# Performance work log

Hardware: AMD Instinct MI355X
Metric: run time of the kernel (lower is better)

Reference implementation:

```python
import jax, jax.numpy as jnp
import numpy as np

IN_F = 4096
OUT_F = 11008
GROUP_SIZE = 128
BITS = 4
PACK = 32 // BITS  # 8 uint4 nibbles per int32


def _unpack_uint4(packed):
    # packed: (rows, cols) int32 -> (rows, cols*8) int32 nibbles in [0,15]
    shifts = (jnp.arange(PACK, dtype=jnp.int32) * BITS)[None, None, :]
    nib = (packed[:, :, None] >> shifts) & 15
    return nib.reshape(packed.shape[0], packed.shape[1] * PACK)


def _dequant(qweight, qzeros, scales):
    # Mirrors torch.ops.hpu.convert_from_uint4: w = (uint4 - zp) * scale,
    # group-wise along the in_features dimension (rows).
    w = _unpack_uint4(qweight).astype(scales.dtype)          # (IN_F, OUT_F)
    zp = _unpack_uint4(qzeros).astype(scales.dtype)          # (n_groups, OUT_F)
    sc_full = jnp.repeat(scales, GROUP_SIZE, axis=0)          # (IN_F, OUT_F)
    zp_full = jnp.repeat(zp, GROUP_SIZE, axis=0)              # (IN_F, OUT_F)
    return (w - zp_full) * sc_full


def setup_inputs() -> dict:
    key = jax.random.key(0)
    k1, k2, k3, k4 = jax.random.split(key, 4)
    n_groups = IN_F // GROUP_SIZE
    inp = jax.random.normal(k1, (2, 2048, IN_F), dtype=jnp.float32)
    qweight = jax.random.randint(k2, (IN_F, OUT_F // PACK), 0, 2147483647, dtype=jnp.int32)
    qzeros = jax.random.randint(k3, (n_groups, OUT_F // PACK), 0, 2147483647, dtype=jnp.int32)
    scales = jax.random.uniform(k4, (n_groups, OUT_F), dtype=jnp.float32) * 0.01 + 1e-3
    return {"input": inp, "qweight": qweight, "qzeros": qzeros, "scales": scales}


def reference(input, qweight, qzeros, scales):
    weight = _dequant(qweight, qzeros, scales)                # (IN_F, OUT_F)
    out = jnp.einsum('bsi,io->bso', input, weight)            # (B, S, OUT_F)
    return out.astype(input.dtype)
```

## Files before the change

kernel.cpp:

```cpp
#include <hip/hip_runtime.h>
#include <stdint.h>

#define IN_F   4096
#define OUT_F  11008
#define QCOLS  (OUT_F / 8)
#define NGRP   32
#define M_TOT  4096

typedef __attribute__((ext_vector_type(8))) short short8;
typedef __attribute__((ext_vector_type(4))) float floatx4;

__device__ __forceinline__ short f2bf(float f) {
    union { float f; uint32_t u; } v; v.f = f;
    uint32_t u = v.u;
    u += 0x7FFFu + ((u >> 16) & 1u);
    return (short)(u >> 16);
}

__global__ __launch_bounds__(256)
void dequant_kernel(const int* __restrict__ qw, const int* __restrict__ qz,
                    const float* __restrict__ scl, short* __restrict__ wt)
{
    const int t    = blockIdx.x * 256 + threadIdx.x;
    const int c    = t % QCOLS;
    const int kblk = t / QCOLS;
    const int k0   = kblk << 5;
    const int g    = kblk >> 2;

    uint32_t q[32];
    const int* qp = qw + (size_t)k0 * QCOLS + c;
    #pragma unroll
    for (int kk = 0; kk < 32; ++kk) q[kk] = (uint32_t)qp[(size_t)kk * QCOLS];

    const uint32_t z = (uint32_t)qz[g * QCOLS + c];
    const float* sp = scl + (size_t)g * OUT_F + c * 8;
    const float4 s0 = *(const float4*)sp;
    const float4 s1 = *(const float4*)(sp + 4);
    const float sc8[8] = {s0.x, s0.y, s0.z, s0.w, s1.x, s1.y, s1.z, s1.w};

    #pragma unroll
    for (int j = 0; j < 8; ++j) {
        const int sh = j << 2;
        const float sc = sc8[j];
        const float zo = -(float)((z >> sh) & 15u) * sc;
        short8 o0, o1, o2, o3;
        #pragma unroll
        for (int kk = 0; kk < 8; ++kk) {
            o0[kk] = f2bf(fmaf((float)((q[kk]      >> sh) & 15u), sc, zo));
            o1[kk] = f2bf(fmaf((float)((q[kk + 8]  >> sh) & 15u), sc, zo));
            o2[kk] = f2bf(fmaf((float)((q[kk + 16] >> sh) & 15u), sc, zo));
            o3[kk] = f2bf(fmaf((float)((q[kk + 24] >> sh) & 15u), sc, zo));
        }
        short* dst = wt + (size_t)(c * 8 + j) * IN_F + k0;
        *(short8*)(dst)      = o0;
        *(short8*)(dst + 8)  = o1;
        *(short8*)(dst + 16) = o2;
        *(short8*)(dst + 24) = o3;
    }
}

__global__ __launch_bounds__(256)
void cast_kernel(const float* __restrict__ A, short* __restrict__ Ab)
{
    const size_t i = ((size_t)blockIdx.x * 256 + threadIdx.x) * 8;
    const float4 a0 = *(const float4*)(A + i);
    const float4 a1 = *(const float4*)(A + i + 4);
    short8 o;
    o[0] = f2bf(a0.x); o[1] = f2bf(a0.y); o[2] = f2bf(a0.z); o[3] = f2bf(a0.w);
    o[4] = f2bf(a1.x); o[5] = f2bf(a1.y); o[6] = f2bf(a1.z); o[7] = f2bf(a1.w);
    *(short8*)(Ab + i) = o;
}

#define GBK 64

__global__ __launch_bounds__(256, 3)
void gemm_kernel(const short* __restrict__ Ab, const short* __restrict__ Bt,
                 float* __restrict__ out)
{
    __shared__ short As[128 * GBK];
    __shared__ short Bs[128 * GBK];

    const int tid  = threadIdx.x;
    const int lane = tid & 63;
    const int w    = tid >> 6;
    const int m0   = blockIdx.y * 128;
    const int n0   = blockIdx.x * 128;

    const int srow = lane >> 3;
    const int kseg = (lane & 7) ^ srow;
    const short* agp[4];
    const short* bgp[4];
    short* alp[4];
    short* blp[4];
    #pragma unroll
    for (int s = 0; s < 4; ++s) {
        const int slot = w * 4 + s;
        const int row  = slot * 8 + srow;
        agp[s] = Ab + (size_t)(m0 + row) * IN_F + kseg * 8;
        bgp[s] = Bt + (size_t)(n0 + row) * IN_F + kseg * 8;
        alp[s] = As + slot * 512;
        blp[s] = Bs + slot * 512;
    }

    const int lrow = lane & 15;
    const int quad = lane >> 4;
    const int wm   = ((w >> 1) & 1) << 6;
    const int wn   = (w & 1) << 6;

    int aoff[4], boff[4];
    #pragma unroll
    for (int i = 0; i < 4; ++i) {
        const int swz = (quad ^ (lrow & 7)) * 8;
        aoff[i] = (wm + i * 16 + lrow) * GBK + swz;
        boff[i] = (wn + i * 16 + lrow) * GBK + swz;
    }

    floatx4 acc[4][4];
    #pragma unroll
    for (int i = 0; i < 4; ++i)
        #pragma unroll
        for (int j = 0; j < 4; ++j)
            acc[i][j] = (floatx4)0.f;

    for (int it = 0; it < IN_F / GBK; ++it) {
        __syncthreads();
        #pragma unroll
        for (int s = 0; s < 4; ++s) {
            __builtin_amdgcn_global_load_lds(
                (const __attribute__((address_space(1))) void*)agp[s],
                (__attribute__((address_space(3))) void*)alp[s], 16, 0, 0);
            __builtin_amdgcn_global_load_lds(
                (const __attribute__((address_space(1))) void*)bgp[s],
                (__attribute__((address_space(3))) void*)blp[s], 16, 0, 0);
            agp[s] += GBK;
            bgp[s] += GBK;
        }
        __syncthreads();

        #pragma unroll
        for (int kx = 0; kx < 64; kx += 32) {
            short8 af[4], bf[4];
            #pragma unroll
            for (int mt = 0; mt < 4; ++mt)
                af[mt] = *(const short8*)(As + (aoff[mt] ^ kx));
            #pragma unroll
            for (int nt = 0; nt < 4; ++nt)
                bf[nt] = *(const short8*)(Bs + (boff[nt] ^ kx));
            #pragma unroll
            for (int mt = 0; mt < 4; ++mt)
                #pragma unroll
                for (int nt = 0; nt < 4; ++nt)
                    acc[mt][nt] = __builtin_amdgcn_mfma_f32_16x16x32_bf16(
                        af[mt], bf[nt], acc[mt][nt], 0, 0, 0);
        }
    }

    #pragma unroll
    for (int mt = 0; mt < 4; ++mt) {
        #pragma unroll
        for (int nt = 0; nt < 4; ++nt) {
            const int col = n0 + wn + nt * 16 + lrow;
            float* op = out + (size_t)(m0 + wm + mt * 16 + quad * 4) * OUT_F + col;
            #pragma unroll
            for (int r = 0; r < 4; ++r)
                op[(size_t)r * OUT_F] = acc[mt][nt][r];
        }
    }
}

#define BM 128
#define BN 128
#define LDA 40
#define LDB 40

__global__ __launch_bounds__(256, 2)
void wql_kernel(const float* __restrict__ A,
                const int*   __restrict__ qw,
                const int*   __restrict__ qz,
                const float* __restrict__ scl,
                float*       __restrict__ out)
{
    __shared__ short As[BM * LDA];
    __shared__ short Bs[BN * LDB];

    const int tid = threadIdx.x;
    const int m0  = blockIdx.y * BM;
    const int n0  = blockIdx.x * BN;

    const int a_row  = tid >> 1;
    const int a_kseg = (tid & 1) << 4;
    const float* a_base = A + (size_t)(m0 + a_row) * IN_F + a_kseg;
    short* a_wr = &As[a_row * LDA + a_kseg];

    const int b_n     = tid & 127;
    const int b_khalf = (tid >> 7) << 4;
    const int c_glob  = (n0 >> 3) + (b_n >> 3);
    const int shift   = (b_n & 7) << 2;
    short* b_wr = &Bs[b_n * LDB + b_khalf];

    const int lane = tid & 63;
    const int wm   = ((tid >> 7) & 1) << 6;
    const int wn   = ((tid >> 6) & 1) << 6;
    const int lrow = lane & 15;
    const int quad = lane >> 4;

    const short* a_rd = &As[(wm + lrow) * LDA + quad * 8];
    const short* b_rd = &Bs[(wn + lrow) * LDB + quad * 8];

    floatx4 acc[4][4];
    #pragma unroll
    for (int i = 0; i < 4; ++i)
        #pragma unroll
        for (int j = 0; j < 4; ++j)
            acc[i][j] = (floatx4)0.f;

    for (int g = 0; g < NGRP; ++g) {
        const uint32_t z  = (uint32_t)qz[g * QCOLS + c_glob];
        const float    sc = scl[g * OUT_F + n0 + b_n];
        const float    zo = -(float)((z >> shift) & 15u) * sc;

        #pragma unroll 1
        for (int t4 = 0; t4 < 4; ++t4) {
            const int k0 = (g << 7) + (t4 << 5);
            const float4* ap = (const float4*)(a_base + k0);
            float4 av0 = ap[0], av1 = ap[1], av2 = ap[2], av3 = ap[3];

            const int* qp = qw + (size_t)(k0 + b_khalf) * QCOLS + c_glob;
            uint32_t qv[16];
            #pragma unroll
            for (int kk = 0; kk < 16; ++kk) qv[kk] = (uint32_t)qp[kk * QCOLS];

            __syncthreads();

            short8 aw0, aw1;
            aw0[0]=f2bf(av0.x); aw0[1]=f2bf(av0.y); aw0[2]=f2bf(av0.z); aw0[3]=f2bf(av0.w);
            aw0[4]=f2bf(av1.x); aw0[5]=f2bf(av1.y); aw0[6]=f2bf(av1.z); aw0[7]=f2bf(av1.w);
            aw1[0]=f2bf(av2.x); aw1[1]=f2bf(av2.y); aw1[2]=f2bf(av2.z); aw1[3]=f2bf(av2.w);
            aw1[4]=f2bf(av3.x); aw1[5]=f2bf(av3.y); aw1[6]=f2bf(av3.z); aw1[7]=f2bf(av3.w);
            *(short8*)a_wr       = aw0;
            *(short8*)(a_wr + 8) = aw1;

            short8 bw0, bw1;
            #pragma unroll
            for (int kk = 0; kk < 8; ++kk)
                bw0[kk] = f2bf(fmaf((float)((qv[kk] >> shift) & 15u), sc, zo));
            #pragma unroll
            for (int kk = 0; kk < 8; ++kk)
                bw1[kk] = f2bf(fmaf((float)((qv[8 + kk] >> shift) & 15u), sc, zo));
            *(short8*)b_wr       = bw0;
            *(short8*)(b_wr + 8) = bw1;

            __syncthreads();

            short8 af[4], bf[4];
            #pragma unroll
            for (int mt = 0; mt < 4; ++mt)
                af[mt] = *(const short8*)(a_rd + mt * 16 * LDA);
            #pragma unroll
            for (int nt = 0; nt < 4; ++nt)
                bf[nt] = *(const short8*)(b_rd + nt * 16 * LDB);

            #pragma unroll
            for (int mt = 0; mt < 4; ++mt)
                #pragma unroll
                for (int nt = 0; nt < 4; ++nt)
                    acc[mt][nt] = __builtin_amdgcn_mfma_f32_16x16x32_bf16(
                        af[mt], bf[nt], acc[mt][nt], 0, 0, 0);
        }
    }

    #pragma unroll
    for (int mt = 0; mt < 4; ++mt) {
        #pragma unroll
        for (int nt = 0; nt < 4; ++nt) {
            const int col = n0 + wn + nt * 16 + lrow;
            float* op = out + (size_t)(m0 + wm + mt * 16 + quad * 4) * OUT_F + col;
            #pragma unroll
            for (int r = 0; r < 4; ++r)
                op[(size_t)r * OUT_F] = acc[mt][nt][r];
        }
    }
}

extern "C" void kernel_launch(void* const* d_in, const int* in_sizes, int n_in,
                              void* d_out, int out_size, void* d_ws, size_t ws_size,
                              hipStream_t stream) {
    const float* input   = (const float*)d_in[0];
    const int*   qweight = (const int*)d_in[1];
    const int*   qzeros  = (const int*)d_in[2];
    const float* scales  = (const float*)d_in[3];
    float*       out     = (float*)d_out;

    const size_t WT_BYTES = (size_t)OUT_F * IN_F * 2;
    const size_t AB_BYTES = (size_t)M_TOT * IN_F * 2;

    if (ws_size >= WT_BYTES + AB_BYTES) {
        short* wt = (short*)d_ws;
        short* ab = (short*)((char*)d_ws + WT_BYTES);

        dequant_kernel<<<(QCOLS * 128) / 256, 256, 0, stream>>>(qweight, qzeros, scales, wt);
        cast_kernel<<<(size_t)M_TOT * IN_F / 8 / 256, 256, 0, stream>>>(input, ab);
        dim3 grid(OUT_F / 128, M_TOT / 128);
        gemm_kernel<<<grid, 256, 0, stream>>>(ab, wt, out);
    } else {
        dim3 grid(OUT_F / BN, M_TOT / BM);
        wql_kernel<<<grid, 256, 0, stream>>>(input, qweight, qzeros, scales, out);
    }
}
```

Measured before the change: 728.1 us.

## Restructure dequant via LDS staging and swap GEMM grid order

The dequant kernel now stages a 64x32 tile of packed weights in LDS. Each thread produces one output column over 64 k-values and writes 128 contiguous bytes, instead of each thread doing 32 strided global loads and writing 8 separate rows. The GEMM grid is transposed so consecutive blocks walk along M while sharing the same N tile of weights, which changes L2 reuse between the activation and weight operands. This adds LDS traffic and a barrier in dequant, and the new block order may hurt reuse of the activation tiles.

```diff
diff --git a/kernel.cpp b/kernel.cpp
--- a/kernel.cpp
+++ b/kernel.cpp
@@ -21,42 +21,44 @@
 void dequant_kernel(const int* __restrict__ qw, const int* __restrict__ qz,
                     const float* __restrict__ scl, short* __restrict__ wt)
 {
-    const int t    = blockIdx.x * 256 + threadIdx.x;
-    const int c    = t % QCOLS;
-    const int kblk = t / QCOLS;
-    const int k0   = kblk << 5;
-    const int g    = kblk >> 2;
-
-    uint32_t q[32];
-    const int* qp = qw + (size_t)k0 * QCOLS + c;
-    #pragma unroll
-    for (int kk = 0; kk < 32; ++kk) q[kk] = (uint32_t)qp[(size_t)kk * QCOLS];
-
-    const uint32_t z = (uint32_t)qz[g * QCOLS + c];
-    const float* sp = scl + (size_t)g * OUT_F + c * 8;
-    const float4 s0 = *(const float4*)sp;
-    const float4 s1 = *(const float4*)(sp + 4);
-    const float sc8[8] = {s0.x, s0.y, s0.z, s0.w, s1.x, s1.y, s1.z, s1.w};
-
-    #pragma unroll
-    for (int j = 0; j < 8; ++j) {
-        const int sh = j << 2;
-        const float sc = sc8[j];
-        const float zo = -(float)((z >> sh) & 15u) * sc;
-        short8 o0, o1, o2, o3;
+    __shared__ int qlds[64 * 32];
+
+    const int tid = threadIdx.x;
+    const int nb  = blockIdx.x;
+    const int kb  = blockIdx.y;
+    const int n0  = nb * 256;
+    const int c0  = nb * 32;
+    const int k0  = kb * 64;
+    const int g   = kb >> 1;
+
+    #pragma unroll
+    for (int i = 0; i < 8; ++i) {
+        const int f = tid + i * 256;
+        const int k = f >> 5, c = f & 31;
+        qlds[f] = qw[(size_t)(k0 + k) * QCOLS + c0 + c];
+    }
+    __syncthreads();
+
+    const int   cl = tid >> 3;
+    const int   sh = (tid & 7) << 2;
+    const uint32_t z  = (uint32_t)qz[(size_t)g * QCOLS + c0 + cl];
+    const float sc = scl[(size_t)g * OUT_F + n0 + tid];
+    const float zo = -(float)((z >> sh) & 15u) * sc;
+
+    short8 o[8];
+    #pragma unroll
+    for (int i = 0; i < 8; ++i) {
         #pragma unroll
         for (int kk = 0; kk < 8; ++kk) {
-            o0[kk] = f2bf(fmaf((float)((q[kk]      >> sh) & 15u), sc, zo));
-            o1[kk] = f2bf(fmaf((float)((q[kk + 8]  >> sh) & 15u), sc, zo));
-            o2[kk] = f2bf(fmaf((float)((q[kk + 16] >> sh) & 15u), sc, zo));
-            o3[kk] = f2bf(fmaf((float)((q[kk + 24] >> sh) & 15u), sc, zo));
-        }
-        short* dst = wt + (size_t)(c * 8 + j) * IN_F + k0;
-        *(short8*)(dst)      = o0;
-        *(short8*)(dst + 8)  = o1;
-        *(short8*)(dst + 16) = o2;
-        *(short8*)(dst + 24) = o3;
-    }
+            const uint32_t q = (uint32_t)qlds[(i * 8 + kk) * 32 + cl];
+            o[i][kk] = f2bf(fmaf((float)((q >> sh) & 15u), sc, zo));
+        }
+    }
+
+    short* dst = wt + (size_t)(n0 + tid) * IN_F + k0;
+    #pragma unroll
+    for (int i = 0; i < 8; ++i)
+        *(short8*)(dst + i * 8) = o[i];
 }
 
 __global__ __launch_bounds__(256)
@@ -83,8 +85,8 @@
     const int tid  = threadIdx.x;
     const int lane = tid & 63;
     const int w    = tid >> 6;
-    const int m0   = blockIdx.y * 128;
-    const int n0   = blockIdx.x * 128;
+    const int m0   = blockIdx.x * 128;
+    const int n0   = blockIdx.y * 128;
 
     const int srow = lane >> 3;
     const int kseg = (lane & 7) ^ srow;
@@ -298,9 +300,10 @@
         short* wt = (short*)d_ws;
         short* ab = (short*)((char*)d_ws + WT_BYTES);
 
-        dequant_kernel<<<(QCOLS * 128) / 256, 256, 0, stream>>>(qweight, qzeros, scales, wt);
+        dim3 dq_grid(OUT_F / 256, IN_F / 64);
+        dequant_kernel<<<dq_grid, 256, 0, stream>>>(qweight, qzeros, scales, wt);
         cast_kernel<<<(size_t)M_TOT * IN_F / 8 / 256, 256, 0, stream>>>(input, ab);
-        dim3 grid(OUT_F / 128, M_TOT / 128);
+        dim3 grid(M_TOT / 128, OUT_F / 128);
         gemm_kernel<<<grid, 256, 0, stream>>>(ab, wt, out);
     } else {
         dim3 grid(OUT_F / BN, M_TOT / BM);
```

Result: faster. 607.9 us (-16.5%).
